# Kernel optimization log

Measured on AMD Instinct MI355X. Metric: run time of the kernel, lower is better.

Reference implementation:

```python
import jax, jax.numpy as jnp
import numpy as np
from jax import lax

EPS = 1e-07
B, NPRIM, NSEC, DP, DS = 512, 1152, 10, 8, 16


def setup_inputs() -> dict:
    key = jax.random.key(0)
    ks = jax.random.split(key, 12)
    inp = {}
    inp['x'] = jax.random.uniform(ks[0], (B, 28, 28, 1), dtype=jnp.float32)
    inp['labels'] = jax.random.randint(ks[1], (B,), 0, NSEC)
    # conv1: 9x9, 1 -> 256, relu ; conv2 (primary caps): 9x9 stride2, 256 -> 256
    inp['conv1_k'] = jax.random.normal(ks[2], (9, 9, 1, 256), dtype=jnp.float32) * 0.05
    inp['conv1_b'] = jnp.zeros((256,), dtype=jnp.float32)
    inp['conv2_k'] = jax.random.normal(ks[3], (9, 9, 256, 256), dtype=jnp.float32) * 0.02
    inp['conv2_b'] = jnp.zeros((256,), dtype=jnp.float32)
    # pose transform W: [1152, 10, 16, 8]
    inp['w'] = jax.random.normal(ks[4], (NPRIM, NSEC, DS, DP), dtype=jnp.float32) * 0.05
    # decoder
    inp['d1_w'] = jax.random.normal(ks[5], (NSEC * DS, 512), dtype=jnp.float32) * 0.05
    inp['d1_b'] = jnp.zeros((512,), dtype=jnp.float32)
    inp['d2_w'] = jax.random.normal(ks[6], (512, 1024), dtype=jnp.float32) * 0.05
    inp['d2_b'] = jnp.zeros((1024,), dtype=jnp.float32)
    inp['d3_w'] = jax.random.normal(ks[7], (1024, 784), dtype=jnp.float32) * 0.05
    inp['d3_b'] = jnp.zeros((784,), dtype=jnp.float32)
    return inp


def _conv(x, k, b, stride):
    y = lax.conv_general_dilated(x, k, (stride, stride), 'VALID',
                                 dimension_numbers=('NHWC', 'HWIO', 'NHWC'))
    return y + b


def _squash(s):
    # s: [..., D]
    s_norm = jnp.linalg.norm(s, axis=-1, keepdims=True)
    sq = jnp.square(s_norm)
    return sq / (1.0 + sq) * s / (s_norm + EPS)


def reference(x, labels, conv1_k, conv1_b, conv2_k, conv2_b, w,
              d1_w, d1_b, d2_w, d2_b, d3_w, d3_b):
    h = jax.nn.relu(_conv(x, conv1_k, conv1_b, 1))        # [B,20,20,256]
    p = _conv(h, conv2_k, conv2_b, 2)                      # [B,6,6,256]
    u = p.reshape(x.shape[0], NPRIM, DP)                   # [B,1152,8]
    # u_hat[b,n,s,d] = sum_p w[n,s,d,p] * u[b,n,p]
    u_hat = jnp.einsum('nsdp,bnp->bnsd', w, u)             # [B,1152,10,16]

    b_logits = jnp.zeros((x.shape[0], NPRIM, NSEC, 1), dtype=u_hat.dtype)
    v = None
    for _ in range(3):  # r routing iterations (fixed, small)
        c = jax.nn.softmax(b_logits, axis=-2)              # softmax over 10 secondary caps
        s = jnp.sum(c * u_hat, axis=1, keepdims=True)      # [B,1,10,16]
        v = _squash(s)                                     # [B,1,10,16]
        agreement = jnp.sum(u_hat * v, axis=-1, keepdims=True)  # [B,1152,10,1]
        b_logits = b_logits + agreement

    y = jax.nn.one_hot(labels, NSEC, dtype=v.dtype)        # [B,10]
    mask = y[:, None, :, None]                             # [B,1,10,1]
    v_masked = mask * v
    v_flat = v_masked.reshape(-1, NSEC * DS)               # [B,160]
    r1 = jax.nn.relu(v_flat @ d1_w + d1_b)
    r2 = jax.nn.relu(r1 @ d2_w + d2_b)
    recon = jax.nn.sigmoid(r2 @ d3_w + d3_b)               # [B,784]
    return v, recon
```

## Files before the change

kernel.cpp:

```cpp
#include <hip/hip_runtime.h>

#define USH unsigned short

__device__ inline float bf2f(USH u){ return __uint_as_float(((unsigned)u)<<16); }
__device__ inline USH f2bf(float f){
  unsigned u = __float_as_uint(f);
  return (USH)((u + 0x7FFFu + ((u>>16)&1u))>>16);
}

typedef __attribute__((ext_vector_type(8))) short bf16x8;
typedef __attribute__((ext_vector_type(4))) float f32x4;

__device__ inline void gll16(const USH* g, USH* l){
  __builtin_amdgcn_global_load_lds((const __attribute__((address_space(1))) void*)g,
                                   (__attribute__((address_space(3))) void*)l, 16, 0, 0);
}

__global__ __launch_bounds__(256) void im2col_k(
    const float* __restrict__ x, USH* __restrict__ xcol)
{
  int b = blockIdx.x, t = threadIdx.x;
  __shared__ float xs[784];
  for (int i = t; i < 784; i += 256) xs[i] = x[b*784 + i];
  __syncthreads();
  USH* dst = xcol + (size_t)b*38400;
  for (int idx = t; idx < 38400; idx += 256) {
    int sp = idx / 96, k = idx - sp*96;
    int y = sp / 20, xx = sp - y*20;
    USH v = 0;
    if (k < 81) {
      int dy = k / 9, dx = k - dy*9;
      v = f2bf(xs[(y+dy)*28 + xx + dx]);
    }
    dst[idx] = v;
  }
}

__global__ __launch_bounds__(256) void tr_k1(const float* __restrict__ k1, USH* __restrict__ k1T)
{
  int n = threadIdx.x;
  for (int k = 0; k < 96; ++k)
    k1T[n*96 + k] = (k < 81) ? f2bf(k1[k*256 + n]) : (USH)0;
}

__global__ __launch_bounds__(256) void gemm1(
    const USH* __restrict__ xcol, const USH* __restrict__ k1T,
    const float* __restrict__ b1, USH* __restrict__ h)
{
  int t = threadIdx.x;
  int m0 = blockIdx.x * 64;
  int lane = t & 63, wave = t >> 6;
  int wn = wave * 64;
  int fr = lane & 15, fq = lane >> 4;

  f32x4 acc[4][4];
#pragma unroll
  for (int i = 0; i < 4; ++i)
#pragma unroll
    for (int j = 0; j < 4; ++j)
#pragma unroll
      for (int r = 0; r < 4; ++r) acc[i][j][r] = 0.f;

#pragma unroll
  for (int kt = 0; kt < 3; ++kt) {
    int kc = kt*32 + fq*8;
    bf16x8 af[4], bg[4];
#pragma unroll
    for (int mf = 0; mf < 4; ++mf)
      af[mf] = *(const bf16x8*)&xcol[(size_t)(m0 + mf*16 + fr)*96 + kc];
#pragma unroll
    for (int nf = 0; nf < 4; ++nf)
      bg[nf] = *(const bf16x8*)&k1T[(size_t)(wn + nf*16 + fr)*96 + kc];
#pragma unroll
    for (int mf = 0; mf < 4; ++mf)
#pragma unroll
      for (int nf = 0; nf < 4; ++nf)
        acc[mf][nf] = __builtin_amdgcn_mfma_f32_16x16x32_bf16(af[mf], bg[nf], acc[mf][nf], 0,0,0);
  }

#pragma unroll
  for (int mf = 0; mf < 4; ++mf)
#pragma unroll
    for (int nf = 0; nf < 4; ++nf) {
      int n = wn + nf*16 + fr;
      float bias = b1[n];
#pragma unroll
      for (int r = 0; r < 4; ++r) {
        int m = m0 + mf*16 + fq*4 + r;
        float v = acc[mf][nf][r] + bias;
        h[(size_t)m*256 + n] = f2bf(v > 0.f ? v : 0.f);
      }
    }
}

__global__ __launch_bounds__(256) void tr_k2(const float* __restrict__ k2, USH* __restrict__ k2T)
{
  __shared__ float tile[32][33];
  int kb = blockIdx.x*32, nb = blockIdx.y*32;
  int tx = threadIdx.x & 31, ty = threadIdx.x >> 5;
#pragma unroll
  for (int r = 0; r < 4; ++r) {
    int k = kb + ty + r*8;
    tile[ty + r*8][tx] = k2[(size_t)k*256 + nb + tx];
  }
  __syncthreads();
#pragma unroll
  for (int r = 0; r < 4; ++r) {
    int n = nb + ty + r*8;
    k2T[(size_t)n*20736 + kb + tx] = f2bf(tile[tx][ty + r*8]);
  }
}

__global__ __launch_bounds__(256) void conv2_mfma(
    const USH* __restrict__ h, const USH* __restrict__ k2T,
    float* __restrict__ up)
{
  __shared__ __align__(16) USH Asm[2][128*64];
  __shared__ __align__(16) USH Bsm[2][64*64];
  int t = threadIdx.x;
  int mb = blockIdx.x, nb = blockIdx.y, ksl = blockIdx.z;

  int sg = (((t&7) ^ ((t>>3)&7)) << 3);

  int arow_off[4];
#pragma unroll
  for (int i = 0; i < 4; ++i) {
    int row = (t>>3) + i*32;
    int m = mb*128 + row;
    int bb = m/36, r = m - bb*36;
    int oy = r/6, ox = r - oy*6;
    arow_off[i] = bb*102400 + oy*10240 + ox*512 + sg;
  }
  int brow_off[2];
#pragma unroll
  for (int i = 0; i < 2; ++i) {
    int nl = (t>>3) + i*32;
    brow_off[i] = (nb*64 + nl)*20736 + sg;
  }

  int lane = t & 63;
  int wave = t >> 6;
  int wm = (wave>>1)*64, wn = (wave&1)*32;
  int fr = lane & 15, fq = lane >> 4;

  f32x4 acc[4][2];
#pragma unroll
  for (int i = 0; i < 4; ++i)
#pragma unroll
    for (int j = 0; j < 2; ++j)
#pragma unroll
      for (int r = 0; r < 4; ++r) acc[i][j][r] = 0.f;

  int rg0 = (((0*4 + fq) ^ (fr&7)) << 3);
  int rg1 = (((1*4 + fq) ^ (fr&7)) << 3);

#define STAGE(buf, kt) do {                                            \
    int j_ = (kt) >> 2;                                                \
    int cin0_ = ((kt) & 3) << 6;                                       \
    int dy_ = j_/9, dx_ = j_ - dy_*9;                                  \
    int koff_ = (dy_*20 + dx_)*256 + cin0_;                            \
    USH* Ad_ = &Asm[buf][(t>>6)*512];                                  \
    USH* Bd_ = &Bsm[buf][(t>>6)*512];                                  \
    _Pragma("unroll")                                                  \
    for (int i_ = 0; i_ < 4; ++i_) gll16(h + arow_off[i_] + koff_, Ad_ + i_*2048); \
    _Pragma("unroll")                                                  \
    for (int i_ = 0; i_ < 2; ++i_) gll16(k2T + brow_off[i_] + (kt)*64, Bd_ + i_*2048); \
  } while(0)

  const int k0 = ksl*162, kend = k0 + 162;
  STAGE(0, k0);
  __syncthreads();

  int cur = 0;
  for (int kt = k0; kt < kend; ++kt) {
    if (kt + 1 < kend) STAGE(cur^1, kt+1);

    bf16x8 af[4][2], bg[2][2];
#pragma unroll
    for (int mf = 0; mf < 4; ++mf) {
      af[mf][0] = *(const bf16x8*)&Asm[cur][(wm + mf*16 + fr)*64 + rg0];
      af[mf][1] = *(const bf16x8*)&Asm[cur][(wm + mf*16 + fr)*64 + rg1];
    }
#pragma unroll
    for (int nf = 0; nf < 2; ++nf) {
      bg[nf][0] = *(const bf16x8*)&Bsm[cur][(wn + nf*16 + fr)*64 + rg0];
      bg[nf][1] = *(const bf16x8*)&Bsm[cur][(wn + nf*16 + fr)*64 + rg1];
    }
#pragma unroll
    for (int mf = 0; mf < 4; ++mf)
#pragma unroll
      for (int nf = 0; nf < 2; ++nf) {
        acc[mf][nf] = __builtin_amdgcn_mfma_f32_16x16x32_bf16(af[mf][0], bg[nf][0], acc[mf][nf], 0,0,0);
        acc[mf][nf] = __builtin_amdgcn_mfma_f32_16x16x32_bf16(af[mf][1], bg[nf][1], acc[mf][nf], 0,0,0);
      }
    __syncthreads();
    cur ^= 1;
  }
#undef STAGE

  float* dst = up + (size_t)ksl*4718592;
#pragma unroll
  for (int mf = 0; mf < 4; ++mf)
#pragma unroll
    for (int nf = 0; nf < 2; ++nf) {
      int n = nb*64 + wn + nf*16 + fr;
#pragma unroll
      for (int r = 0; r < 4; ++r) {
        int m = mb*128 + wm + mf*16 + fq*4 + r;
        dst[(size_t)m*256 + n] = acc[mf][nf][r];
      }
    }
}

__global__ __launch_bounds__(256) void reduce_u(
    const float* __restrict__ up, const float* __restrict__ b2, float* __restrict__ u)
{
  int i = blockIdx.x*256 + threadIdx.x;
  f32x4 a = *(const f32x4*)&up[(size_t)i*4];
  f32x4 b = *(const f32x4*)&up[4718592ull + (size_t)i*4];
  int n0 = (i*4) & 255;
  f32x4 o;
#pragma unroll
  for (int j = 0; j < 4; ++j) o[j] = a[j] + b[j] + b2[n0 + j];
  *(f32x4*)&u[(size_t)i*4] = o;
}

__global__ __launch_bounds__(192) void wsum_tr(const float* __restrict__ w,
    float* __restrict__ Ws)
{
  int n = blockIdx.x, t = threadIdx.x;
  __shared__ float wn[1280];
  for (int i = t; i < 1280; i += 192) wn[i] = w[n*1280 + i];
  __syncthreads();
  if (t < 160) {
#pragma unroll
    for (int p = 0; p < 8; ++p)
      Ws[((size_t)n*8 + p)*160 + t] = wn[(t>>4)*128 + (t&15)*8 + p];
  }
}

__global__ __launch_bounds__(192) void p1gemm(const float* __restrict__ u,
    const float* __restrict__ Ws, float* __restrict__ part)
{
  int b0 = blockIdx.x*32, k0 = blockIdx.y*288;
  int t = threadIdx.x;
  __shared__ float usm[288*36];
  for (int i = t; i < 288*32; i += 192) {
    int bl = i/288, kk = i - bl*288;
    usm[kk*36 + bl] = u[(size_t)(b0+bl)*9216 + k0 + kk];
  }
  __syncthreads();
  if (t < 160) {
    const float* wp = Ws + (size_t)k0*160 + t;
#pragma unroll 1
    for (int half = 0; half < 2; ++half) {
      float acc[16];
#pragma unroll
      for (int i = 0; i < 16; ++i) acc[i] = 0.f;
      for (int kk = 0; kk < 288; ++kk) {
        float wv = wp[(size_t)kk*160];
        const f32x4* ub = (const f32x4*)&usm[kk*36 + half*16];
        f32x4 u0 = ub[0], u1 = ub[1], u2 = ub[2], u3 = ub[3];
#pragma unroll
        for (int i = 0; i < 4; ++i) {
          acc[i]    += u0[i]*wv;
          acc[4+i]  += u1[i]*wv;
          acc[8+i]  += u2[i]*wv;
          acc[12+i] += u3[i]*wv;
        }
      }
      float* pp = &part[((size_t)blockIdx.y*512 + b0 + half*16)*160 + t];
#pragma unroll
      for (int i = 0; i < 16; ++i) pp[(size_t)i*160] = acc[i];
    }
  }
}

__global__ __launch_bounds__(192) void squash1(const float* __restrict__ part,
    float* __restrict__ vout)
{
  int b = blockIdx.x, t = threadIdx.x;
  if (t < 160) {
    float sv = 0.f;
    for (int ks = 0; ks < 32; ++ks) sv += part[((size_t)ks*512 + b)*160 + t];
    sv *= 0.1f;
    float n2 = sv*sv;
    n2 += __shfl_xor(n2, 1, 16);
    n2 += __shfl_xor(n2, 2, 16);
    n2 += __shfl_xor(n2, 4, 16);
    n2 += __shfl_xor(n2, 8, 16);
    float nrm = sqrtf(n2);
    float o = (n2/(1.f + n2)) * sv / (nrm + 1e-7f);
    vout[b*160 + t] = o;
  }
}

__global__ __launch_bounds__(256) void uhat_kernel(
    const float* __restrict__ u, const float* __restrict__ w, USH* __restrict__ uh)
{
  int n = blockIdx.x, b0 = blockIdx.y*64;
  int t = threadIdx.x;
  __shared__ float wsm[20*65];
  __shared__ float usm[512];
  for (int i = t; i < 1280; i += 256) wsm[(i>>6)*65 + (i&63)] = w[n*1280 + i];
  for (int i = t; i < 512; i += 256) {
    int bl = i>>3, p = i&7;
    usm[i] = u[(size_t)(b0+bl)*9216 + n*8 + p];
  }
  __syncthreads();
  for (int v = t; v < 1280; v += 256) {
    int bl = v/20, oct = v - bl*20;
    const float* upt = &usm[bl*8];
    bf16x8 pk;
#pragma unroll
    for (int j = 0; j < 8; ++j) {
      const float* wp = &wsm[oct*65 + j*8];
      float a = 0.f;
#pragma unroll
      for (int p = 0; p < 8; ++p) a += wp[p]*upt[p];
      pk[j] = (short)f2bf(a);
    }
    *(bf16x8*)&uh[(size_t)(b0+bl)*184320 + n*160 + oct*8] = pk;
  }
}

template<int PASS>
__global__ __launch_bounds__(256) void route_part(
    const USH* __restrict__ uh, const float* __restrict__ vin,
    float* __restrict__ L, float* __restrict__ partR)
{
  int b = blockIdx.x, nc = blockIdx.y;
  int t = threadIdx.x;
  int lane = t & 63, w = t >> 6;
  int grp = lane >> 4, s = lane & 15;
  int stream = w*4 + grp;
  bool act = s < 10;

  float vr[16];
  {
    const float* vp = vin + b*160 + s*16;
#pragma unroll
    for (int d = 0; d < 16; ++d) vr[d] = act ? vp[d] : 0.f;
  }
  float acc[16];
#pragma unroll
  for (int d = 0; d < 16; ++d) acc[d] = 0.f;

  const USH* ub = uh + (size_t)b*184320;
  int nbase = nc*288 + stream*18;
  for (int ni = 0; ni < 18; ++ni) {
    int n = nbase + ni;
    float uv[16];
    if (act) {
      const USH* upt = ub + n*160 + s*16;
      bf16x8 p0 = *(const bf16x8*)upt;
      bf16x8 p1 = *(const bf16x8*)(upt + 8);
#pragma unroll
      for (int d = 0; d < 8; ++d) { uv[d] = bf2f((USH)p0[d]); uv[8+d] = bf2f((USH)p1[d]); }
    } else {
#pragma unroll
      for (int d = 0; d < 16; ++d) uv[d] = 0.f;
    }

    float dot = 0.f;
#pragma unroll
    for (int d = 0; d < 16; ++d) dot += uv[d]*vr[d];
    float lg;
    if (PASS == 2) {
      lg = dot;
      if (act) L[((size_t)b*1152 + n)*10 + s] = dot;
    } else {
      lg = act ? (L[((size_t)b*1152 + n)*10 + s] + dot) : 0.f;
    }
    if (!act) lg = -1e30f;
    float mx = lg;
    mx = fmaxf(mx, __shfl_xor(mx, 1, 16));
    mx = fmaxf(mx, __shfl_xor(mx, 2, 16));
    mx = fmaxf(mx, __shfl_xor(mx, 4, 16));
    mx = fmaxf(mx, __shfl_xor(mx, 8, 16));
    float e = __expf(lg - mx);
    float sum = e;
    sum += __shfl_xor(sum, 1, 16);
    sum += __shfl_xor(sum, 2, 16);
    sum += __shfl_xor(sum, 4, 16);
    sum += __shfl_xor(sum, 8, 16);
    float c = e / sum;
#pragma unroll
    for (int d = 0; d < 16; ++d) acc[d] += c*uv[d];
  }

  __shared__ float red[16][168];
  if (act) {
#pragma unroll
    for (int d = 0; d < 16; ++d) red[stream][s*16 + d] = acc[d];
  }
  __syncthreads();
  if (t < 160) {
    float sv = 0.f;
#pragma unroll
    for (int k = 0; k < 16; ++k) sv += red[k][t];
    partR[((size_t)nc*512 + b)*160 + t] = sv;
  }
}

template<int PASS>
__global__ __launch_bounds__(192) void squash_part(const float* __restrict__ partR,
    float* __restrict__ vout, float* __restrict__ vext)
{
  int b = blockIdx.x, t = threadIdx.x;
  if (t < 160) {
    float sv = 0.f;
#pragma unroll
    for (int nc = 0; nc < 4; ++nc) sv += partR[((size_t)nc*512 + b)*160 + t];
    float n2 = sv*sv;
    n2 += __shfl_xor(n2, 1, 16);
    n2 += __shfl_xor(n2, 2, 16);
    n2 += __shfl_xor(n2, 4, 16);
    n2 += __shfl_xor(n2, 8, 16);
    float nrm = sqrtf(n2);
    float o = (n2/(1.f + n2)) * sv / (nrm + 1e-7f);
    vout[b*160 + t] = o;
    if (PASS == 3) vext[b*160 + t] = o;
  }
}

__global__ __launch_bounds__(512) void d1_kernel(const float* __restrict__ v3,
    const int* __restrict__ labels, const float* __restrict__ w,
    const float* __restrict__ bias, float* __restrict__ r1)
{
  int b = blockIdx.x; int j = threadIdx.x;
  int lb = labels[b];
  float acc = bias[j];
#pragma unroll
  for (int d = 0; d < 16; ++d)
    acc += v3[b*160 + lb*16 + d] * w[(lb*16 + d)*512 + j];
  r1[(size_t)b*512 + j] = acc > 0.f ? acc : 0.f;
}

__global__ __launch_bounds__(256) void d2_kernel(const float* __restrict__ a,
    const float* __restrict__ w, const float* __restrict__ bias, float* __restrict__ o)
{
  int j = blockIdx.x*256 + threadIdx.x;
  int b0 = blockIdx.y*4;
  __shared__ float as[4*512];
  for (int i = threadIdx.x; i < 4*512; i += 256) as[i] = a[(size_t)(b0 + (i>>9))*512 + (i&511)];
  __syncthreads();
  float acc[4];
  float bs = bias[j];
#pragma unroll
  for (int i = 0; i < 4; ++i) acc[i] = bs;
  for (int k = 0; k < 512; ++k) {
    float wv = w[(size_t)k*1024 + j];
#pragma unroll
    for (int i = 0; i < 4; ++i) acc[i] += as[i*512 + k]*wv;
  }
#pragma unroll
  for (int i = 0; i < 4; ++i)
    o[(size_t)(b0+i)*1024 + j] = acc[i] > 0.f ? acc[i] : 0.f;
}

__global__ __launch_bounds__(256) void d3_kernel(const float* __restrict__ a,
    const float* __restrict__ w, const float* __restrict__ bias, float* __restrict__ o)
{
  int j = blockIdx.x*256 + threadIdx.x;
  int b0 = blockIdx.y*4;
  __shared__ float as[4*1024];
  for (int i = threadIdx.x; i < 4*1024; i += 256) as[i] = a[(size_t)(b0 + (i>>10))*1024 + (i&1023)];
  __syncthreads();
  if (j < 784) {
    float acc[4];
    float bs = bias[j];
#pragma unroll
    for (int i = 0; i < 4; ++i) acc[i] = bs;
    for (int k = 0; k < 1024; ++k) {
      float wv = w[(size_t)k*784 + j];
#pragma unroll
      for (int i = 0; i < 4; ++i) acc[i] += as[i*1024 + k]*wv;
    }
#pragma unroll
    for (int i = 0; i < 4; ++i)
      o[(size_t)(b0+i)*784 + j] = 1.f/(1.f + __expf(-acc[i]));
  }
}

extern "C" void kernel_launch(void* const* d_in, const int* in_sizes, int n_in,
                              void* d_out, int out_size, void* d_ws, size_t ws_size,
                              hipStream_t stream)
{
  const float* x   = (const float*)d_in[0];
  const int*   lab = (const int*)  d_in[1];
  const float* k1  = (const float*)d_in[2];
  const float* b1  = (const float*)d_in[3];
  const float* k2  = (const float*)d_in[4];
  const float* b2  = (const float*)d_in[5];
  const float* w   = (const float*)d_in[6];
  const float* d1w = (const float*)d_in[7];
  const float* d1b = (const float*)d_in[8];
  const float* d2w = (const float*)d_in[9];
  const float* d2b = (const float*)d_in[10];
  const float* d3w = (const float*)d_in[11];
  const float* d3b = (const float*)d_in[12];
  float* out = (float*)d_out;

  char* ws = (char*)d_ws;
  USH*   uh    = (USH*)(ws + 0);
  USH*   h     = (USH*)(ws + 0);
  float* up    = (float*)(ws + 104857600ull);
  USH*   xcol  = (USH*)(ws + 142606336ull);
  float* u     = (float*)(ws + 188743680ull);
  USH*   k2T   = (USH*)(ws + 207618048ull);
  float* part  = (float*)(ws + 207618048ull);
  float* partR = (float*)(ws + 207618048ull);
  float* L     = (float*)(ws + 218234880ull);
  float* Wsum  = (float*)(ws + 218234880ull);
  USH*   k1T   = (USH*)(ws + 241827840ull);
  float* v1    = (float*)(ws + 242155520ull);
  float* v2    = (float*)(ws + 242483200ull);
  float* v3    = (float*)(ws + 242810880ull);
  float* r1    = (float*)(ws + 243138560ull);
  float* r2    = (float*)(ws + 244187136ull);

  im2col_k<<<512, 256, 0, stream>>>(x, xcol);
  tr_k1<<<1, 256, 0, stream>>>(k1, k1T);
  gemm1<<<3200, 256, 0, stream>>>(xcol, k1T, b1, h);

  tr_k2<<<dim3(648,8), 256, 0, stream>>>(k2, k2T);
  conv2_mfma<<<dim3(144,4,2), 256, 0, stream>>>(h, k2T, up);
  reduce_u<<<4608, 256, 0, stream>>>(up, b2, u);

  wsum_tr<<<1152, 192, 0, stream>>>(w, Wsum);
  p1gemm<<<dim3(16,32), 192, 0, stream>>>(u, Wsum, part);
  squash1<<<512, 192, 0, stream>>>(part, v1);

  uhat_kernel<<<dim3(1152,8), 256, 0, stream>>>(u, w, uh);

  route_part<2><<<dim3(512,4), 256, 0, stream>>>(uh, v1, L, partR);
  squash_part<2><<<512, 192, 0, stream>>>(partR, v2, nullptr);
  route_part<3><<<dim3(512,4), 256, 0, stream>>>(uh, v2, L, partR);
  squash_part<3><<<512, 192, 0, stream>>>(partR, v3, out);

  d1_kernel<<<512, 512, 0, stream>>>(v3, lab, d1w, d1b, r1);
  d2_kernel<<<dim3(4,128), 256, 0, stream>>>(r1, d2w, d2b, r2);
  d3_kernel<<<dim3(4,128), 256, 0, stream>>>(r2, d3w, d3b, out + 81920);
}
```

Baseline: 712.8 us.

## Recompute u_hat on the fly in fused routing kernels instead of materializing it

Replaces the separate u_hat materialization (bf16 buffer of about 190MB) and the p1gemm path with a route_fuse kernel that recomputes u_hat from u and W in registers for each routing pass, then does the dot, softmax and accumulation in the same kernel. This removes the large u_hat write and the two reads of it, as well as the bf16 rounding, at the cost of recomputing the W·u products three times and adding more block-level syncs per primary capsule. Partial sums now span 72 groups, so the squash kernel reduces over 72 slices.

```diff
diff --git a/kernel.cpp b/kernel.cpp
--- a/kernel.cpp
+++ b/kernel.cpp
@@ -225,193 +225,136 @@
   *(f32x4*)&u[(size_t)i*4] = o;
 }
 
-__global__ __launch_bounds__(192) void wsum_tr(const float* __restrict__ w,
-    float* __restrict__ Ws)
-{
-  int n = blockIdx.x, t = threadIdx.x;
-  __shared__ float wn[1280];
-  for (int i = t; i < 1280; i += 192) wn[i] = w[n*1280 + i];
-  __syncthreads();
-  if (t < 160) {
-#pragma unroll
-    for (int p = 0; p < 8; ++p)
-      Ws[((size_t)n*8 + p)*160 + t] = wn[(t>>4)*128 + (t&15)*8 + p];
-  }
-}
-
-__global__ __launch_bounds__(192) void p1gemm(const float* __restrict__ u,
-    const float* __restrict__ Ws, float* __restrict__ part)
-{
-  int b0 = blockIdx.x*32, k0 = blockIdx.y*288;
+template<int PASS>
+__global__ __launch_bounds__(256, 3) void route_fuse(
+    const float* __restrict__ u, const float* __restrict__ w,
+    const float* __restrict__ vin, float* __restrict__ L,
+    float* __restrict__ partR)
+{
+  int ng = blockIdx.x, bc = blockIdx.y;
+  int n0 = ng*16, b0 = bc*64;
   int t = threadIdx.x;
-  __shared__ float usm[288*36];
-  for (int i = t; i < 288*32; i += 192) {
-    int bl = i/288, kk = i - bl*288;
-    usm[kk*36 + bl] = u[(size_t)(b0+bl)*9216 + k0 + kk];
-  }
-  __syncthreads();
-  if (t < 160) {
-    const float* wp = Ws + (size_t)k0*160 + t;
-#pragma unroll 1
-    for (int half = 0; half < 2; ++half) {
-      float acc[16];
-#pragma unroll
-      for (int i = 0; i < 16; ++i) acc[i] = 0.f;
-      for (int kk = 0; kk < 288; ++kk) {
-        float wv = wp[(size_t)kk*160];
-        const f32x4* ub = (const f32x4*)&usm[kk*36 + half*16];
-        f32x4 u0 = ub[0], u1 = ub[1], u2 = ub[2], u3 = ub[3];
-#pragma unroll
-        for (int i = 0; i < 4; ++i) {
-          acc[i]    += u0[i]*wv;
-          acc[4+i]  += u1[i]*wv;
-          acc[8+i]  += u2[i]*wv;
-          acc[12+i] += u3[i]*wv;
+
+  __shared__ float u_lds[64][132];
+  __shared__ float wsm[20*68];
+  __shared__ float dotp[64][20];
+  __shared__ float csm[64][12];
+
+  for (int i = t; i < 64*128; i += 256) {
+    int bl = i >> 7, off = i & 127;
+    u_lds[bl][off] = u[(size_t)(b0+bl)*9216 + n0*8 + off];
+  }
+
+  int bl_[5], oct_[5];
+#pragma unroll
+  for (int r = 0; r < 5; ++r) {
+    int v = r*256 + t;
+    bl_[r] = v/20; oct_[r] = v - bl_[r]*20;
+  }
+
+  float vr_[5][8];
+  if (PASS >= 2) {
+#pragma unroll
+    for (int r = 0; r < 5; ++r) {
+      const float* vp = vin + (size_t)(b0+bl_[r])*160 + oct_[r]*8;
+#pragma unroll
+      for (int j = 0; j < 8; ++j) vr_[r][j] = vp[j];
+    }
+  }
+
+  float acc_[5][8];
+#pragma unroll
+  for (int r = 0; r < 5; ++r)
+#pragma unroll
+    for (int j = 0; j < 8; ++j) acc_[r][j] = 0.f;
+
+  for (int ni = 0; ni < 16; ++ni) {
+    int n = n0 + ni;
+    __syncthreads();
+    for (int i = t; i < 1280; i += 256) {
+      int oct = i >> 6, off = i & 63;
+      wsm[oct*68 + off] = w[(size_t)n*1280 + i];
+    }
+    __syncthreads();
+
+    float uh_[5][8];
+#pragma unroll
+    for (int r = 0; r < 5; ++r) {
+      const f32x4* wp = (const f32x4*)&wsm[oct_[r]*68];
+      const f32x4* upt = (const f32x4*)&u_lds[bl_[r]][ni*8];
+      f32x4 u0 = upt[0], u1 = upt[1];
+      float pd = 0.f;
+#pragma unroll
+      for (int j = 0; j < 8; ++j) {
+        f32x4 wa = wp[2*j], wb = wp[2*j+1];
+        float hh = wa[0]*u0[0]+wa[1]*u0[1]+wa[2]*u0[2]+wa[3]*u0[3]
+                 + wb[0]*u1[0]+wb[1]*u1[1]+wb[2]*u1[2]+wb[3]*u1[3];
+        uh_[r][j] = hh;
+        if (PASS >= 2) pd += hh * vr_[r][j];
+      }
+      if (PASS >= 2) dotp[bl_[r]][oct_[r]] = pd;
+    }
+
+    if (PASS == 1) {
+#pragma unroll
+      for (int r = 0; r < 5; ++r)
+#pragma unroll
+        for (int j = 0; j < 8; ++j) acc_[r][j] += uh_[r][j];
+    } else {
+      __syncthreads();
+      if (t < 64) {
+        float dt[10];
+#pragma unroll
+        for (int s = 0; s < 10; ++s) dt[s] = dotp[t][2*s] + dotp[t][2*s+1];
+        size_t lb = ((size_t)n*512 + b0 + t)*10;
+        if (PASS == 2) {
+#pragma unroll
+          for (int s = 0; s < 10; ++s) L[lb + s] = dt[s];
+        } else {
+#pragma unroll
+          for (int s = 0; s < 10; ++s) dt[s] += L[lb + s];
         }
-      }
-      float* pp = &part[((size_t)blockIdx.y*512 + b0 + half*16)*160 + t];
-#pragma unroll
-      for (int i = 0; i < 16; ++i) pp[(size_t)i*160] = acc[i];
-    }
-  }
-}
-
-__global__ __launch_bounds__(192) void squash1(const float* __restrict__ part,
-    float* __restrict__ vout)
+        float mx = dt[0];
+#pragma unroll
+        for (int s = 1; s < 10; ++s) mx = fmaxf(mx, dt[s]);
+        float es[10];
+        float sum = 0.f;
+#pragma unroll
+        for (int s = 0; s < 10; ++s) { es[s] = __expf(dt[s]-mx); sum += es[s]; }
+        float inv = 1.f/sum;
+#pragma unroll
+        for (int s = 0; s < 10; ++s) csm[t][s] = es[s]*inv;
+      }
+      __syncthreads();
+#pragma unroll
+      for (int r = 0; r < 5; ++r) {
+        float c = csm[bl_[r]][oct_[r] >> 1];
+#pragma unroll
+        for (int j = 0; j < 8; ++j) acc_[r][j] += c*uh_[r][j];
+      }
+    }
+  }
+
+#pragma unroll
+  for (int r = 0; r < 5; ++r) {
+    float* pp = &partR[((size_t)ng*512 + b0 + bl_[r])*160 + oct_[r]*8];
+    f32x4 o0, o1;
+#pragma unroll
+    for (int j = 0; j < 4; ++j) { o0[j] = acc_[r][j]; o1[j] = acc_[r][4+j]; }
+    *(f32x4*)pp = o0;
+    *(f32x4*)(pp+4) = o1;
+  }
+}
+
+template<int PASS>
+__global__ __launch_bounds__(192) void squash72(const float* __restrict__ partR,
+    float* __restrict__ vout, float* __restrict__ vext)
 {
   int b = blockIdx.x, t = threadIdx.x;
   if (t < 160) {
     float sv = 0.f;
-    for (int ks = 0; ks < 32; ++ks) sv += part[((size_t)ks*512 + b)*160 + t];
-    sv *= 0.1f;
-    float n2 = sv*sv;
-    n2 += __shfl_xor(n2, 1, 16);
-    n2 += __shfl_xor(n2, 2, 16);
-    n2 += __shfl_xor(n2, 4, 16);
-    n2 += __shfl_xor(n2, 8, 16);
-    float nrm = sqrtf(n2);
-    float o = (n2/(1.f + n2)) * sv / (nrm + 1e-7f);
-    vout[b*160 + t] = o;
-  }
-}
-
-__global__ __launch_bounds__(256) void uhat_kernel(
-    const float* __restrict__ u, const float* __restrict__ w, USH* __restrict__ uh)
-{
-  int n = blockIdx.x, b0 = blockIdx.y*64;
-  int t = threadIdx.x;
-  __shared__ float wsm[20*65];
-  __shared__ float usm[512];
-  for (int i = t; i < 1280; i += 256) wsm[(i>>6)*65 + (i&63)] = w[n*1280 + i];
-  for (int i = t; i < 512; i += 256) {
-    int bl = i>>3, p = i&7;
-    usm[i] = u[(size_t)(b0+bl)*9216 + n*8 + p];
-  }
-  __syncthreads();
-  for (int v = t; v < 1280; v += 256) {
-    int bl = v/20, oct = v - bl*20;
-    const float* upt = &usm[bl*8];
-    bf16x8 pk;
-#pragma unroll
-    for (int j = 0; j < 8; ++j) {
-      const float* wp = &wsm[oct*65 + j*8];
-      float a = 0.f;
-#pragma unroll
-      for (int p = 0; p < 8; ++p) a += wp[p]*upt[p];
-      pk[j] = (short)f2bf(a);
-    }
-    *(bf16x8*)&uh[(size_t)(b0+bl)*184320 + n*160 + oct*8] = pk;
-  }
-}
-
-template<int PASS>
-__global__ __launch_bounds__(256) void route_part(
-    const USH* __restrict__ uh, const float* __restrict__ vin,
-    float* __restrict__ L, float* __restrict__ partR)
-{
-  int b = blockIdx.x, nc = blockIdx.y;
-  int t = threadIdx.x;
-  int lane = t & 63, w = t >> 6;
-  int grp = lane >> 4, s = lane & 15;
-  int stream = w*4 + grp;
-  bool act = s < 10;
-
-  float vr[16];
-  {
-    const float* vp = vin + b*160 + s*16;
-#pragma unroll
-    for (int d = 0; d < 16; ++d) vr[d] = act ? vp[d] : 0.f;
-  }
-  float acc[16];
-#pragma unroll
-  for (int d = 0; d < 16; ++d) acc[d] = 0.f;
-
-  const USH* ub = uh + (size_t)b*184320;
-  int nbase = nc*288 + stream*18;
-  for (int ni = 0; ni < 18; ++ni) {
-    int n = nbase + ni;
-    float uv[16];
-    if (act) {
-      const USH* upt = ub + n*160 + s*16;
-      bf16x8 p0 = *(const bf16x8*)upt;
-      bf16x8 p1 = *(const bf16x8*)(upt + 8);
-#pragma unroll
-      for (int d = 0; d < 8; ++d) { uv[d] = bf2f((USH)p0[d]); uv[8+d] = bf2f((USH)p1[d]); }
-    } else {
-#pragma unroll
-      for (int d = 0; d < 16; ++d) uv[d] = 0.f;
-    }
-
-    float dot = 0.f;
-#pragma unroll
-    for (int d = 0; d < 16; ++d) dot += uv[d]*vr[d];
-    float lg;
-    if (PASS == 2) {
-      lg = dot;
-      if (act) L[((size_t)b*1152 + n)*10 + s] = dot;
-    } else {
-      lg = act ? (L[((size_t)b*1152 + n)*10 + s] + dot) : 0.f;
-    }
-    if (!act) lg = -1e30f;
-    float mx = lg;
-    mx = fmaxf(mx, __shfl_xor(mx, 1, 16));
-    mx = fmaxf(mx, __shfl_xor(mx, 2, 16));
-    mx = fmaxf(mx, __shfl_xor(mx, 4, 16));
-    mx = fmaxf(mx, __shfl_xor(mx, 8, 16));
-    float e = __expf(lg - mx);
-    float sum = e;
-    sum += __shfl_xor(sum, 1, 16);
-    sum += __shfl_xor(sum, 2, 16);
-    sum += __shfl_xor(sum, 4, 16);
-    sum += __shfl_xor(sum, 8, 16);
-    float c = e / sum;
-#pragma unroll
-    for (int d = 0; d < 16; ++d) acc[d] += c*uv[d];
-  }
-
-  __shared__ float red[16][168];
-  if (act) {
-#pragma unroll
-    for (int d = 0; d < 16; ++d) red[stream][s*16 + d] = acc[d];
-  }
-  __syncthreads();
-  if (t < 160) {
-    float sv = 0.f;
-#pragma unroll
-    for (int k = 0; k < 16; ++k) sv += red[k][t];
-    partR[((size_t)nc*512 + b)*160 + t] = sv;
-  }
-}
-
-template<int PASS>
-__global__ __launch_bounds__(192) void squash_part(const float* __restrict__ partR,
-    float* __restrict__ vout, float* __restrict__ vext)
-{
-  int b = blockIdx.x, t = threadIdx.x;
-  if (t < 160) {
-    float sv = 0.f;
-#pragma unroll
-    for (int nc = 0; nc < 4; ++nc) sv += partR[((size_t)nc*512 + b)*160 + t];
+    for (int ngr = 0; ngr < 72; ++ngr) sv += partR[((size_t)ngr*512 + b)*160 + t];
+    if (PASS == 1) sv *= 0.1f;
     float n2 = sv*sv;
     n2 += __shfl_xor(n2, 1, 16);
     n2 += __shfl_xor(n2, 2, 16);
@@ -503,16 +446,13 @@
   float* out = (float*)d_out;
 
   char* ws = (char*)d_ws;
-  USH*   uh    = (USH*)(ws + 0);
   USH*   h     = (USH*)(ws + 0);
   float* up    = (float*)(ws + 104857600ull);
+  float* partR = (float*)(ws + 104857600ull);
   USH*   xcol  = (USH*)(ws + 142606336ull);
   float* u     = (float*)(ws + 188743680ull);
   USH*   k2T   = (USH*)(ws + 207618048ull);
-  float* part  = (float*)(ws + 207618048ull);
-  float* partR = (float*)(ws + 207618048ull);
   float* L     = (float*)(ws + 218234880ull);
-  float* Wsum  = (float*)(ws + 218234880ull);
   USH*   k1T   = (USH*)(ws + 241827840ull);
   float* v1    = (float*)(ws + 242155520ull);
   float* v2    = (float*)(ws + 242483200ull);
@@ -528,16 +468,12 @@
   conv2_mfma<<<dim3(144,4,2), 256, 0, stream>>>(h, k2T, up);
   reduce_u<<<4608, 256, 0, stream>>>(up, b2, u);
 
-  wsum_tr<<<1152, 192, 0, stream>>>(w, Wsum);
-  p1gemm<<<dim3(16,32), 192, 0, stream>>>(u, Wsum, part);
-  squash1<<<512, 192, 0, stream>>>(part, v1);
-
-  uhat_kernel<<<dim3(1152,8), 256, 0, stream>>>(u, w, uh);
-
-  route_part<2><<<dim3(512,4), 256, 0, stream>>>(uh, v1, L, partR);
-  squash_part<2><<<512, 192, 0, stream>>>(partR, v2, nullptr);
-  route_part<3><<<dim3(512,4), 256, 0, stream>>>(uh, v2, L, partR);
-  squash_part<3><<<512, 192, 0, stream>>>(partR, v3, out);
+  route_fuse<1><<<dim3(72,8), 256, 0, stream>>>(u, w, nullptr, nullptr, partR);
+  squash72<1><<<512, 192, 0, stream>>>(partR, v1, nullptr);
+  route_fuse<2><<<dim3(72,8), 256, 0, stream>>>(u, w, v1, L, partR);
+  squash72<2><<<512, 192, 0, stream>>>(partR, v2, nullptr);
+  route_fuse<3><<<dim3(72,8), 256, 0, stream>>>(u, w, v2, L, partR);
+  squash72<3><<<512, 192, 0, stream>>>(partR, v3, out);
 
   d1_kernel<<<512, 512, 0, stream>>>(v3, lab, d1w, d1b, r1);
   d2_kernel<<<dim3(4,128), 256, 0, stream>>>(r1, d2w, d2b, r2);
```

Result: slower. 750.5 us (+5.3%).
